# Performance work log

Measured on AMD Instinct MI355X. Metric: run time of the kernel, lower is better.

The kernel has to match this reference:

```python
import jax, jax.numpy as jnp
import numpy as np

WS = 8      # window size
NH = 8      # num heads
SCALE = 4.0 # qk_scale=4 from module defaults
GK = 9      # gaze depthwise kernel (nw=8 even -> 9)
EPS = 1e-5


def _rel_pos_index(ws):
    coords = np.stack(np.meshgrid(np.arange(ws), np.arange(ws), indexing='ij'))
    cf = coords.reshape(2, -1)
    rel = (cf[:, :, None] - cf[:, None, :]).transpose(1, 2, 0).astype(np.int64)
    rel[..., 0] += ws - 1
    rel[..., 1] += ws - 1
    rel[..., 0] *= 2 * ws - 1
    return jnp.asarray(rel.sum(-1))  # (N, N)


def _ln(x, g, b):
    m = x.mean(-1, keepdims=True)
    v = ((x - m) ** 2).mean(-1, keepdims=True)
    return (x - m) / jnp.sqrt(v + EPS) * g + b


def _forward(x, norm1_g, norm1_b, qkv_w, qkv_b, rpb_table, proj_w, proj_b,
             gaze_w, gaze_b, norm2_g, norm2_b, fc1_w, fc1_b, fc2_w, fc2_b, H, W):
    B, C, _, _ = x.shape
    hd = C // NH
    nw = H // WS           # windows per side (= Fold dilation)
    N = WS * WS            # tokens per window
    xf = x.transpose(0, 2, 3, 1).reshape(B, H * W, C)
    shortcut = xf
    xn = _ln(xf, norm1_g, norm1_b).reshape(B, H, W, C)
    # window partition -> (B*nw*nw, N, C)
    xw = xn.reshape(B, nw, WS, nw, WS, C).transpose(0, 1, 3, 2, 4, 5).reshape(B * nw * nw, N, C)
    qkv = (xw @ qkv_w.T + qkv_b).reshape(-1, N, 3, NH, hd).transpose(2, 0, 3, 1, 4)
    q, k, v = qkv[0] * SCALE, qkv[1], qkv[2]
    attn = jnp.einsum('whnd,whmd->whnm', q, k)  # (nWin, heads, N, N)
    rpi = _rel_pos_index(WS)
    bias = rpb_table[rpi.reshape(-1)].reshape(N, N, NH).transpose(2, 0, 1)
    attn = jax.nn.softmax(attn + bias[None], axis=-1)
    out = jnp.einsum('whnm,whmd->whnd', attn, v).transpose(0, 2, 1, 3).reshape(-1, N, C)
    # gaze branch: Fold (dilated scatter of windows into image), depthwise conv, Unfold
    v6 = v.reshape(B, nw, nw, NH, WS, WS, hd)          # (B, wh, ww, nh, i, j, hd)
    img = v6.transpose(0, 4, 1, 5, 2, 3, 6).reshape(B, H, W, C)  # row = i*nw+wh, col = j*nw+ww
    pad = GK // 2
    img = jax.lax.conv_general_dilated(
        img, gaze_w, (1, 1), ((pad, pad), (pad, pad)),
        dimension_numbers=('NHWC', 'HWIO', 'NHWC'), feature_group_count=C) + gaze_b
    gz = img.reshape(B, WS, nw, WS, nw, C).transpose(0, 2, 4, 1, 3, 5).reshape(B * nw * nw, N, C)
    out = (out + gz) @ proj_w.T + proj_b
    # window reverse -> (B, H*W, C)
    xr = out.reshape(B, nw, nw, WS, WS, C).transpose(0, 1, 3, 2, 4, 5).reshape(B, H * W, C)
    xf = shortcut + xr
    h = _ln(xf, norm2_g, norm2_b)
    h = jax.nn.gelu(h @ fc1_w.T + fc1_b, approximate=False) @ fc2_w.T + fc2_b
    xf = xf + h
    return xf.reshape(B, H, W, C).transpose(0, 3, 1, 2)


def setup_inputs() -> dict:
    key = jax.random.key(0)
    ks = jax.random.split(key, 8)
    C, H, W, B, HID = 256, 64, 64, 16, 1024
    return {
        'H': 64, 'W': 64,
        'x': jax.random.normal(ks[0], (B, C, H, W), jnp.float32),
        'norm1_g': jnp.ones((C,), jnp.float32),
        'norm1_b': jnp.zeros((C,), jnp.float32),
        'qkv_w': jax.random.normal(ks[1], (3 * C, C), jnp.float32) * 0.02,
        'qkv_b': jnp.zeros((3 * C,), jnp.float32),
        'rpb_table': jax.random.normal(ks[2], (225, NH), jnp.float32) * 0.02,
        'proj_w': jax.random.normal(ks[3], (C, C), jnp.float32) * 0.02,
        'proj_b': jnp.zeros((C,), jnp.float32),
        'gaze_w': jax.random.normal(ks[4], (GK, GK, 1, C), jnp.float32) * 0.02,
        'gaze_b': jnp.zeros((C,), jnp.float32),
        'norm2_g': jnp.ones((C,), jnp.float32),
        'norm2_b': jnp.zeros((C,), jnp.float32),
        'fc1_w': jax.random.normal(ks[5], (HID, C), jnp.float32) * 0.02,
        'fc1_b': jnp.zeros((HID,), jnp.float32),
        'fc2_w': jax.random.normal(ks[6], (C, HID), jnp.float32) * 0.02,
        'fc2_b': jnp.zeros((C,), jnp.float32),
    }


def reference(H, W, x, norm1_g, norm1_b, qkv_w, qkv_b, rpb_table, proj_w, proj_b,
              gaze_w, gaze_b, norm2_g, norm2_b, fc1_w, fc1_b, fc2_w, fc2_b):
    return _forward(x, norm1_g, norm1_b, qkv_w, qkv_b, rpb_table, proj_w, proj_b,
                    gaze_w, gaze_b, norm2_g, norm2_b, fc1_w, fc1_b, fc2_w, fc2_b, H, W)
```

## Files before the change

kernel.cpp:

```cpp
#include <hip/hip_runtime.h>
#include <math.h>

#define BB    16
#define CC    256
#define HH    64
#define WW2   64
#define NHD   8
#define HD    32
#define NT    64
#define NWIN  1024
#define TOK   65536
#define HIDN  1024
#define GKS   9
#define GPAD  4

typedef short bf16x8 __attribute__((ext_vector_type(8)));
typedef float f32x4  __attribute__((ext_vector_type(4)));
typedef unsigned short u16x8 __attribute__((ext_vector_type(8)));

__device__ __forceinline__ float b2f(unsigned short u) {
    return __uint_as_float(((unsigned int)u) << 16);
}
__device__ __forceinline__ unsigned short f2b(float f) {
    unsigned int x = __float_as_uint(f);
    unsigned int r = x + 0x7fffu + ((x >> 16) & 1u);
    return (unsigned short)(r >> 16);
}

__device__ __forceinline__ float gelu_f(float v) {
    const float c = 0.7978845608028654f;
    const float u = c * v * (1.0f + 0.044715f * v * v);
    const float e = __builtin_amdgcn_exp2f(2.8853900817779268f * u);
    const float t = 1.0f - 2.0f * __builtin_amdgcn_rcpf(e + 1.0f);
    return 0.5f * v * (1.0f + t);
}

#define O_N1G  64
#define O_N1B  320
#define O_QKVW 576
#define O_QKVB 197184
#define O_RPB  197952
#define O_PW   199808
#define O_PB   265344
#define O_GW   265600
#define O_GB   286336
#define O_N2G  286592
#define O_N2B  286848
#define O_W1   287104
#define O_B1   549248
#define O_W2   550272
#define O_B2   812416

struct ParTab {
    const void* src[15];
    int n[15];
    int off[15];
};

__global__ __launch_bounds__(256) void k_detect(const unsigned short* __restrict__ x,
                                                int* __restrict__ flag) {
    __shared__ int cnt;
    if (threadIdx.x == 0) cnt = 0;
    __syncthreads();
    const unsigned short u = x[threadIdx.x];
    const int e = (u >> 7) & 0xFF;
    if (e >= 140) atomicAdd(&cnt, 1);
    __syncthreads();
    if (threadIdx.x == 0) *flag = (cnt >= 8) ? 1 : 0;
}

__global__ __launch_bounds__(256) void k_conv_par(ParTab tab,
                                                  const int* __restrict__ flag,
                                                  unsigned short* __restrict__ par) {
    const int t = blockIdx.y;
    const int n = tab.n[t], off = tab.off[t];
    const bool f32 = (*flag != 0);
    for (int i = blockIdx.x * 256 + threadIdx.x; i < n; i += 64 * 256) {
        par[off + i] = f32 ? f2b(((const float*)tab.src[t])[i])
                           : ((const unsigned short*)tab.src[t])[i];
    }
}

__global__ __launch_bounds__(256) void k_pre(const void* __restrict__ xsrc,
                                             const int* __restrict__ flag,
                                             const unsigned short* __restrict__ g,
                                             const unsigned short* __restrict__ bt,
                                             unsigned short* __restrict__ SC,
                                             unsigned short* __restrict__ XN) {
    __shared__ __align__(16) unsigned short xs[256 * 65];
    __shared__ float ps[4][64], ps2[4][64];
    __shared__ float mean_s[64], rstd_s[64];
    const int tid = threadIdx.x;
    const int win = blockIdx.x;
    const int b = win >> 6, wh = (win >> 3) & 7, ww = win & 7;
    const bool f32 = (*flag != 0);

    for (int idx = tid; idx < 16384; idx += 256) {
        const int c = idx >> 6, n = idx & 63;
        const int h = wh * 8 + (n >> 3), w = ww * 8 + (n & 7);
        const size_t o = ((size_t)(b * CC + c) * HH + h) * WW2 + w;
        xs[c * 65 + n] = f32 ? f2b(((const float*)xsrc)[o])
                             : ((const unsigned short*)xsrc)[o];
    }
    __syncthreads();
    {
        const int tok = tid & 63, part = tid >> 6;
        float s = 0.f, s2 = 0.f;
        for (int c = part * 64; c < part * 64 + 64; ++c) {
            const float v = b2f(xs[c * 65 + tok]);
            s += v; s2 += v * v;
        }
        ps[part][tok] = s; ps2[part][tok] = s2;
    }
    __syncthreads();
    if (tid < 64) {
        const float s  = ps[0][tid] + ps[1][tid] + ps[2][tid] + ps[3][tid];
        const float s2 = ps2[0][tid] + ps2[1][tid] + ps2[2][tid] + ps2[3][tid];
        const float mean = s * (1.f / 256.f);
        const float var  = s2 * (1.f / 256.f) - mean * mean;
        mean_s[tid] = mean;
        rstd_s[tid] = rsqrtf(var + 1e-5f);
    }
    __syncthreads();
    for (int idx = tid; idx < 16384; idx += 256) {
        const int n = idx >> 8, c = idx & 255;
        const unsigned short raw = xs[c * 65 + n];
        const float v = (b2f(raw) - mean_s[n]) * rstd_s[n] * b2f(g[c]) + b2f(bt[c]);
        const size_t o = (size_t)(win * NT + n) * CC + c;
        SC[o] = raw;
        XN[o] = f2b(v);
    }
}

template <int KDIM, typename PreF, typename PostF>
__device__ __forceinline__ void gemm128(const unsigned short* __restrict__ A,
                                        const unsigned short* __restrict__ Bw,
                                        PreF pre, PostF post8) {
    __shared__ __align__(16) unsigned short smem[128 * 136];
    unsigned short* As = smem;
    unsigned short* Bs = smem + 8192;
    const int tid = threadIdx.x;
    const int wv = tid >> 6, ln = tid & 63;
    const int wm = wv & 1, wn = wv >> 1;
    const int m0 = blockIdx.x * 128, n0 = blockIdx.y * 128;

    f32x4 acc[4][4] = {};

    const int u = tid;

    for (int kb = 0; kb < KDIM; kb += 64) {
#pragma unroll
        for (int i = 0; i < 4; ++i) {
            const int uu = i * 256 + u;
            const int row = uu >> 3;
            const int c8 = ((uu & 7) ^ (row & 7)) * 8;
            __builtin_amdgcn_global_load_lds(
                (const __attribute__((address_space(1))) unsigned int*)
                    &A[(size_t)(m0 + row) * KDIM + kb + c8],
                (__attribute__((address_space(3))) unsigned int*)&As[uu * 8],
                16, 0, 0);
            __builtin_amdgcn_global_load_lds(
                (const __attribute__((address_space(1))) unsigned int*)
                    &Bw[(size_t)(n0 + row) * KDIM + kb + c8],
                (__attribute__((address_space(3))) unsigned int*)&Bs[uu * 8],
                16, 0, 0);
        }
        __syncthreads();
#pragma unroll
        for (int ks = 0; ks < 2; ++ks) {
            bf16x8 af[4], bf[4];
            const int sl = ks * 4 + (ln >> 4);
#pragma unroll
            for (int t = 0; t < 4; ++t) {
                const int ra = wm * 64 + t * 16 + (ln & 15);
                const int rb = wn * 64 + t * 16 + (ln & 15);
                af[t] = *(const bf16x8*)&As[ra * 64 + ((sl ^ (ra & 7)) * 8)];
                bf[t] = *(const bf16x8*)&Bs[rb * 64 + ((sl ^ (rb & 7)) * 8)];
            }
#pragma unroll
            for (int mt = 0; mt < 4; ++mt)
#pragma unroll
                for (int nt = 0; nt < 4; ++nt)
                    acc[mt][nt] = __builtin_amdgcn_mfma_f32_16x16x32_bf16(af[mt], bf[nt], acc[mt][nt], 0, 0, 0);
        }
        __syncthreads();
    }

    unsigned short* Cs = smem;
#pragma unroll
    for (int mt = 0; mt < 4; ++mt)
#pragma unroll
        for (int nt = 0; nt < 4; ++nt)
#pragma unroll
            for (int r = 0; r < 4; ++r) {
                const int ml = wm * 64 + mt * 16 + (ln >> 4) * 4 + r;
                const int nl = wn * 64 + nt * 16 + (ln & 15);
                Cs[ml * 136 + nl] = f2b(pre(m0 + ml, n0 + nl, acc[mt][nt][r]));
            }
    __syncthreads();
#pragma unroll
    for (int i = 0; i < 8; ++i) {
        const int j = i * 256 + tid;
        const int row = j >> 4, c8 = (j & 15) * 8;
        const u16x8 vals = *(const u16x8*)&Cs[row * 136 + c8];
        post8(m0 + row, n0 + c8, vals);
    }
}

__global__ __launch_bounds__(256) void k_gemm_qkv(const unsigned short* __restrict__ XN,
                                                  const unsigned short* __restrict__ Wq,
                                                  const unsigned short* __restrict__ bq,
                                                  unsigned short* __restrict__ Q,
                                                  unsigned short* __restrict__ K,
                                                  unsigned short* __restrict__ V) {
    gemm128<256>(XN, Wq,
        [&](int m, int n, float v) {
            v += b2f(bq[n]);
            return (n < 256) ? v * 4.0f : v;
        },
        [&](int m, int nb, u16x8 vals) {
            unsigned short* dst = (nb < 256) ? Q : ((nb < 512) ? K : V);
            *(u16x8*)&dst[(size_t)m * CC + (nb & 255)] = vals;
        });
}

__global__ __launch_bounds__(256) void k_attn(const unsigned short* __restrict__ Q,
                                              const unsigned short* __restrict__ K,
                                              const unsigned short* __restrict__ V,
                                              const unsigned short* __restrict__ rpb,
                                              unsigned short* __restrict__ AO) {
    __shared__ __align__(16) unsigned short Pb[64 * 72];
    __shared__ __align__(16) unsigned short Vt[32 * 72];
    const int tid = threadIdx.x, wv = tid >> 6, ln = tid & 63;
    const int win = blockIdx.x, head = blockIdx.y;
    const size_t tbase = (size_t)(win * NT) * CC + head * HD;

    for (int idx = tid; idx < 2048; idx += 256) {
        const int tok = idx >> 5, d = idx & 31;
        Vt[d * 72 + tok] = V[tbase + (size_t)tok * CC + d];
    }

    const bf16x8 a = *(const bf16x8*)&Q[tbase + (size_t)(16 * wv + (ln & 15)) * CC + (ln >> 4) * 8];
    f32x4 accs[4] = {};
#pragma unroll
    for (int f = 0; f < 4; ++f) {
        const bf16x8 b = *(const bf16x8*)&K[tbase + (size_t)(f * 16 + (ln & 15)) * CC + (ln >> 4) * 8];
        accs[f] = __builtin_amdgcn_mfma_f32_16x16x32_bf16(a, b, accs[f], 0, 0, 0);
    }
    const int qloc = (ln >> 4) * 4;
#pragma unroll
    for (int f = 0; f < 4; ++f)
#pragma unroll
        for (int r = 0; r < 4; ++r) {
            const int rr = 16 * wv + qloc + r;
            const int cth = f * 16 + (ln & 15);
            const int bidx = ((rr >> 3) - (cth >> 3) + 7) * 15 + ((rr & 7) - (cth & 7) + 7);
            accs[f][r] += b2f(rpb[bidx * NHD + head]);
        }
#pragma unroll
    for (int r = 0; r < 4; ++r) {
        float m = fmaxf(fmaxf(accs[0][r], accs[1][r]), fmaxf(accs[2][r], accs[3][r]));
#pragma unroll
        for (int o = 1; o <= 8; o <<= 1) m = fmaxf(m, __shfl_xor(m, o));
        float p[4], s = 0.f;
#pragma unroll
        for (int f = 0; f < 4; ++f) { p[f] = expf(accs[f][r] - m); s += p[f]; }
#pragma unroll
        for (int o = 1; o <= 8; o <<= 1) s += __shfl_xor(s, o);
        const float inv = 1.f / s;
#pragma unroll
        for (int f = 0; f < 4; ++f)
            Pb[(16 * wv + qloc + r) * 72 + f * 16 + (ln & 15)] = f2b(p[f] * inv);
    }
    __syncthreads();

    f32x4 acco[2] = {};
#pragma unroll
    for (int kb = 0; kb < 64; kb += 32) {
        const bf16x8 ap = *(const bf16x8*)&Pb[(16 * wv + (ln & 15)) * 72 + kb + (ln >> 4) * 8];
#pragma unroll
        for (int f = 0; f < 2; ++f) {
            const bf16x8 bv = *(const bf16x8*)&Vt[(f * 16 + (ln & 15)) * 72 + kb + (ln >> 4) * 8];
            acco[f] = __builtin_amdgcn_mfma_f32_16x16x32_bf16(ap, bv, acco[f], 0, 0, 0);
        }
    }
#pragma unroll
    for (int f = 0; f < 2; ++f)
#pragma unroll
        for (int r = 0; r < 4; ++r) {
            const int rr = 16 * wv + qloc + r;
            const int d = f * 16 + (ln & 15);
            AO[tbase + (size_t)rr * CC + d] = f2b(acco[f][r]);
        }
}

__global__ __launch_bounds__(256) void k_gaze(const unsigned short* __restrict__ V,
                                              const unsigned short* __restrict__ gw,
                                              const unsigned short* __restrict__ gb,
                                              unsigned short* __restrict__ AO) {
    __shared__ __align__(16) unsigned short ins[24 * 16 * 32];
    __shared__ __align__(16) unsigned short wlds[81 * 32];
    const int tid = threadIdx.x;
    const int c0 = blockIdx.x * 8, r0 = blockIdx.y * 16;
    const int b = blockIdx.z >> 3, head = blockIdx.z & 7;

    for (int idx = tid; idx < 1536; idx += 256) {
        const int pix = idx >> 2, v4 = (idx & 3) * 8;
        const int row = pix >> 4, colL = pix & 15;
        const int rp = r0 + row - GPAD, cp = c0 + colL - GPAD;
        uint4 val = {0, 0, 0, 0};
        if (rp >= 0 && rp < HH && cp >= 0 && cp < WW2) {
            const int win = b * 64 + (rp & 7) * 8 + (cp & 7);
            const int n = (rp >> 3) * 8 + (cp >> 3);
            val = *(const uint4*)&V[(size_t)(win * NT + n) * CC + head * HD + v4];
        }
        *(uint4*)&ins[(row * 16 + colL) * 32 + v4] = val;
    }
    for (int idx = tid; idx < 324; idx += 256) {
        const int k = idx >> 2, v4 = (idx & 3) * 8;
        *(uint4*)&wlds[k * 32 + v4] = *(const uint4*)&gw[k * CC + head * HD + v4];
    }
    __syncthreads();

    const int d = tid & 31;
    const int col = tid >> 5;
    float out[16];
#pragma unroll
    for (int ro = 0; ro < 16; ++ro) out[ro] = 0.f;

#pragma unroll
    for (int dx = 0; dx < GKS; ++dx) {
        float wreg[GKS];
#pragma unroll
        for (int dy = 0; dy < GKS; ++dy)
            wreg[dy] = b2f(wlds[(dy * GKS + dx) * 32 + d]);
        float inreg[24];
#pragma unroll
        for (int ri = 0; ri < 24; ++ri)
            inreg[ri] = b2f(ins[(ri * 16 + col + dx) * 32 + d]);
#pragma unroll
        for (int ro = 0; ro < 16; ++ro)
#pragma unroll
            for (int dy = 0; dy < GKS; ++dy)
                out[ro] = fmaf(inreg[ro + dy], wreg[dy], out[ro]);
    }

    const float bias = b2f(gb[head * HD + d]);
    const int c = c0 + col;
#pragma unroll
    for (int ro = 0; ro < 16; ++ro) {
        const int r = r0 + ro;
        const int win0 = b * 64 + (r & 7) * 8 + (c & 7);
        const int n0 = (r >> 3) * 8 + (c >> 3);
        const size_t o = (size_t)(win0 * NT + n0) * CC + head * HD + d;
        AO[o] = f2b(b2f(AO[o]) + out[ro] + bias);
    }
}

__global__ __launch_bounds__(256) void k_gemm_proj(const unsigned short* __restrict__ AO,
                                                   const unsigned short* __restrict__ Wp,
                                                   const unsigned short* __restrict__ bp,
                                                   const unsigned short* __restrict__ SC,
                                                   unsigned short* __restrict__ X2) {
    gemm128<256>(AO, Wp,
        [&](int m, int n, float v) { return v + b2f(bp[n]); },
        [&](int m, int nb, u16x8 vals) {
            const u16x8 sc = *(const u16x8*)&SC[(size_t)m * CC + nb];
            u16x8 o;
#pragma unroll
            for (int j = 0; j < 8; ++j) o[j] = f2b(b2f(vals[j]) + b2f(sc[j]));
            *(u16x8*)&X2[(size_t)m * CC + nb] = o;
        });
}

__global__ __launch_bounds__(256) void k_ln2(const unsigned short* __restrict__ X2,
                                             const unsigned short* __restrict__ g,
                                             const unsigned short* __restrict__ bt,
                                             unsigned short* __restrict__ X2N) {
    const int wv = threadIdx.x >> 6, ln = threadIdx.x & 63;
    const int t = blockIdx.x * 4 + wv;
    float vals[4];
    float s = 0.f, s2 = 0.f;
#pragma unroll
    for (int k = 0; k < 4; ++k) {
        const float v = b2f(X2[(size_t)t * CC + k * 64 + ln]);
        vals[k] = v; s += v; s2 += v * v;
    }
#pragma unroll
    for (int off = 32; off; off >>= 1) {
        s += __shfl_xor(s, off);
        s2 += __shfl_xor(s2, off);
    }
    const float mean = s * (1.f / 256.f);
    const float rstd = rsqrtf(s2 * (1.f / 256.f) - mean * mean + 1e-5f);
#pragma unroll
    for (int k = 0; k < 4; ++k) {
        const int c = k * 64 + ln;
        X2N[(size_t)t * CC + c] = f2b((vals[k] - mean) * rstd * b2f(g[c]) + b2f(bt[c]));
    }
}

__global__ __launch_bounds__(256) void k_gemm_fc1(const unsigned short* __restrict__ X2N,
                                                  const unsigned short* __restrict__ W1,
                                                  const unsigned short* __restrict__ b1,
                                                  unsigned short* __restrict__ H1) {
    gemm128<256>(X2N, W1,
        [&](int m, int n, float v) {
            v += b2f(b1[n]);
            return gelu_f(v);
        },
        [&](int m, int nb, u16x8 vals) {
            *(u16x8*)&H1[(size_t)m * HIDN + nb] = vals;
        });
}

__global__ __launch_bounds__(256) void k_gemm_fc2(const unsigned short* __restrict__ H1,
                                                  const unsigned short* __restrict__ W2,
                                                  const unsigned short* __restrict__ b2v,
                                                  const unsigned short* __restrict__ X2,
                                                  unsigned short* __restrict__ XOUT) {
    gemm128<1024>(H1, W2,
        [&](int m, int n, float v) { return v + b2f(b2v[n]); },
        [&](int m, int nb, u16x8 vals) {
            const u16x8 r = *(const u16x8*)&X2[(size_t)m * CC + nb];
            u16x8 o;
#pragma unroll
            for (int j = 0; j < 8; ++j) o[j] = f2b(b2f(vals[j]) + b2f(r[j]));
            *(u16x8*)&XOUT[(size_t)m * CC + nb] = o;
        });
}

__global__ __launch_bounds__(256) void k_out(const unsigned short* __restrict__ XOUT,
                                             const int* __restrict__ flag,
                                             void* __restrict__ out) {
    __shared__ __align__(16) unsigned short ys[64 * 257];
    const int tid = threadIdx.x;
    const int win = blockIdx.x;
    const int b = win >> 6, wh = (win >> 3) & 7, ww = win & 7;
    for (int idx = tid; idx < 16384; idx += 256) {
        const int n = idx >> 8, c = idx & 255;
        ys[n * 257 + c] = XOUT[(size_t)(win * NT + n) * CC + c];
    }
    __syncthreads();
    const bool f32 = (*flag != 0);
    for (int idx = tid; idx < 16384; idx += 256) {
        const int ch = idx >> 6, n = idx & 63;
        const int h = wh * 8 + (n >> 3), w = ww * 8 + (n & 7);
        const size_t o = ((size_t)(b * CC + ch) * HH + h) * WW2 + w;
        const unsigned short v = ys[n * 257 + ch];
        if (f32) ((float*)out)[o] = b2f(v);
        else     ((unsigned short*)out)[o] = v;
    }
}

extern "C" void kernel_launch(void* const* d_in, const int* in_sizes, int n_in,
                              void* d_out, int out_size, void* d_ws, size_t ws_size,
                              hipStream_t stream) {
    char* ws = (char*)d_ws;
    const size_t MB = 1048576;
    unsigned short* SC  = (unsigned short*)(ws);
    unsigned short* XN  = (unsigned short*)(ws + 32 * MB);
    unsigned short* Qb  = (unsigned short*)(ws + 64 * MB);
    unsigned short* Kb  = (unsigned short*)(ws + 96 * MB);
    unsigned short* Vb  = (unsigned short*)(ws + 128 * MB);
    unsigned short* AO  = (unsigned short*)(ws + 160 * MB);
    unsigned short* H1  = (unsigned short*)(ws + 64 * MB);
    unsigned short* X2  = (unsigned short*)(ws + 192 * MB);
    unsigned short* PAR = (unsigned short*)(ws + 224 * MB);
    int* FLAG = (int*)(ws + 224 * MB);
    unsigned short* X2N  = XN;
    unsigned short* XOUT = XN;

    ParTab tab;
    const int srcidx[15] = {3, 4, 5, 6, 7, 8, 9, 10, 11, 12, 13, 14, 15, 16, 17};
    const int sizes[15]  = {256, 256, 196608, 768, 1800, 65536, 256, 20736, 256,
                            256, 256, 262144, 1024, 262144, 256};
    const int offs[15]   = {O_N1G, O_N1B, O_QKVW, O_QKVB, O_RPB, O_PW, O_PB, O_GW, O_GB,
                            O_N2G, O_N2B, O_W1, O_B1, O_W2, O_B2};
    for (int i = 0; i < 15; ++i) {
        tab.src[i] = d_in[srcidx[i]];
        tab.n[i] = sizes[i];
        tab.off[i] = offs[i];
    }

    k_detect   <<<1,                 256, 0, stream>>>((const unsigned short*)d_in[2], FLAG);
    k_conv_par <<<dim3(64, 15),      256, 0, stream>>>(tab, FLAG, PAR);
    k_pre      <<<NWIN,              256, 0, stream>>>(d_in[2], FLAG, PAR + O_N1G, PAR + O_N1B, SC, XN);
    k_gemm_qkv <<<dim3(512, 6),      256, 0, stream>>>(XN, PAR + O_QKVW, PAR + O_QKVB, Qb, Kb, Vb);
    k_attn     <<<dim3(NWIN, NHD),   256, 0, stream>>>(Qb, Kb, Vb, PAR + O_RPB, AO);
    k_gaze     <<<dim3(8, 4, 128),   256, 0, stream>>>(Vb, PAR + O_GW, PAR + O_GB, AO);
    k_gemm_proj<<<dim3(512, 2),      256, 0, stream>>>(AO, PAR + O_PW, PAR + O_PB, SC, X2);
    k_ln2      <<<TOK / 4,           256, 0, stream>>>(X2, PAR + O_N2G, PAR + O_N2B, X2N);
    k_gemm_fc1 <<<dim3(512, 8),      256, 0, stream>>>(X2N, PAR + O_W1, PAR + O_B1, H1);
    k_gemm_fc2 <<<dim3(512, 2),      256, 0, stream>>>(H1, PAR + O_W2, PAR + O_B2, X2, XOUT);
    k_out      <<<NWIN,              256, 0, stream>>>(XOUT, FLAG, d_out);
}
```

Before: 587.5 us.

## Fold qk scale into weights, hoist GEMM bias, swap grid order, vectorize LN2

Pre-multiplies the Q rows of the QKV weights and bias by the scale during parameter conversion, so the GEMM epilogue no longer multiplies. Hoists the bias load into registers per wave, uses packed v_cvt_pk_bf16 conversions, and uses a cheaper sigmoid-form GELU approximation. Swaps the GEMM grid so the N tiles vary fastest, which should improve reuse of the A tile in L2. Vectorizes the V transpose load in attention and the LN2 kernel to 16-byte accesses. Pre-scaling in bf16 rounds slightly differently, and the GELU form changes numerics a little.

```diff
diff --git a/kernel.cpp b/kernel.cpp
--- a/kernel.cpp
+++ b/kernel.cpp
@@ -26,13 +26,29 @@
     unsigned int r = x + 0x7fffu + ((x >> 16) & 1u);
     return (unsigned short)(r >> 16);
 }
+__device__ __forceinline__ unsigned int cvt_pk_bf16(float lo, float hi) {
+    unsigned int r;
+    asm("v_cvt_pk_bf16_f32 %0, %1, %2" : "=v"(r) : "v"(lo), "v"(hi));
+    return r;
+}
 
 __device__ __forceinline__ float gelu_f(float v) {
-    const float c = 0.7978845608028654f;
-    const float u = c * v * (1.0f + 0.044715f * v * v);
-    const float e = __builtin_amdgcn_exp2f(2.8853900817779268f * u);
-    const float t = 1.0f - 2.0f * __builtin_amdgcn_rcpf(e + 1.0f);
-    return 0.5f * v * (1.0f + t);
+    const float w = v * v;
+    const float u = v * fmaf(w, -0.1029432f, -2.3022082f);
+    const float e = __builtin_amdgcn_exp2f(u);
+    return v * __builtin_amdgcn_rcpf(1.0f + e);
+}
+
+__device__ __forceinline__ u16x8 add_bf8(u16x8 a, u16x8 b) {
+    u16x8 o;
+#pragma unroll
+    for (int j = 0; j < 8; j += 2) {
+        const unsigned int p = cvt_pk_bf16(b2f(a[j]) + b2f(b[j]),
+                                           b2f(a[j + 1]) + b2f(b[j + 1]));
+        o[j] = (unsigned short)p;
+        o[j + 1] = (unsigned short)(p >> 16);
+    }
+    return o;
 }
 
 #define O_N1G  64
@@ -75,9 +91,19 @@
     const int t = blockIdx.y;
     const int n = tab.n[t], off = tab.off[t];
     const bool f32 = (*flag != 0);
+    const bool scaled = (t == 2) || (t == 3);
+    const int slim = (t == 2) ? 65536 : 256;
     for (int i = blockIdx.x * 256 + threadIdx.x; i < n; i += 64 * 256) {
-        par[off + i] = f32 ? f2b(((const float*)tab.src[t])[i])
-                           : ((const unsigned short*)tab.src[t])[i];
+        unsigned short r;
+        if (f32) {
+            float v = ((const float*)tab.src[t])[i];
+            if (scaled && i < slim) v *= 4.0f;
+            r = f2b(v);
+        } else {
+            r = ((const unsigned short*)tab.src[t])[i];
+            if (scaled && i < slim) r = f2b(b2f(r) * 4.0f);
+        }
+        par[off + i] = r;
     }
 }
 
@@ -132,20 +158,25 @@
     }
 }
 
-template <int KDIM, typename PreF, typename PostF>
+template <int KDIM, int ACT, typename PostF>
 __device__ __forceinline__ void gemm128(const unsigned short* __restrict__ A,
                                         const unsigned short* __restrict__ Bw,
-                                        PreF pre, PostF post8) {
+                                        const unsigned short* __restrict__ bias,
+                                        PostF post8) {
     __shared__ __align__(16) unsigned short smem[128 * 136];
     unsigned short* As = smem;
     unsigned short* Bs = smem + 8192;
     const int tid = threadIdx.x;
     const int wv = tid >> 6, ln = tid & 63;
     const int wm = wv & 1, wn = wv >> 1;
-    const int m0 = blockIdx.x * 128, n0 = blockIdx.y * 128;
+    const int m0 = blockIdx.y * 128, n0 = blockIdx.x * 128;
+
+    float bias_v[4];
+#pragma unroll
+    for (int nt = 0; nt < 4; ++nt)
+        bias_v[nt] = b2f(bias[n0 + wn * 64 + nt * 16 + (ln & 15)]);
 
     f32x4 acc[4][4] = {};
-
     const int u = tid;
 
     for (int kb = 0; kb < KDIM; kb += 64) {
@@ -190,13 +221,23 @@
 #pragma unroll
     for (int mt = 0; mt < 4; ++mt)
 #pragma unroll
-        for (int nt = 0; nt < 4; ++nt)
+        for (int nt = 0; nt < 4; ++nt) {
+            float v[4];
 #pragma unroll
             for (int r = 0; r < 4; ++r) {
-                const int ml = wm * 64 + mt * 16 + (ln >> 4) * 4 + r;
-                const int nl = wn * 64 + nt * 16 + (ln & 15);
-                Cs[ml * 136 + nl] = f2b(pre(m0 + ml, n0 + nl, acc[mt][nt][r]));
+                float x = acc[mt][nt][r] + bias_v[nt];
+                if (ACT == 1) x = gelu_f(x);
+                v[r] = x;
             }
+            const int mlb = wm * 64 + mt * 16 + (ln >> 4) * 4;
+            const int nl = wn * 64 + nt * 16 + (ln & 15);
+            const unsigned int p0 = cvt_pk_bf16(v[0], v[1]);
+            const unsigned int p1 = cvt_pk_bf16(v[2], v[3]);
+            Cs[(mlb + 0) * 136 + nl] = (unsigned short)p0;
+            Cs[(mlb + 1) * 136 + nl] = (unsigned short)(p0 >> 16);
+            Cs[(mlb + 2) * 136 + nl] = (unsigned short)p1;
+            Cs[(mlb + 3) * 136 + nl] = (unsigned short)(p1 >> 16);
+        }
     __syncthreads();
 #pragma unroll
     for (int i = 0; i < 8; ++i) {
@@ -213,11 +254,7 @@
                                                   unsigned short* __restrict__ Q,
                                                   unsigned short* __restrict__ K,
                                                   unsigned short* __restrict__ V) {
-    gemm128<256>(XN, Wq,
-        [&](int m, int n, float v) {
-            v += b2f(bq[n]);
-            return (n < 256) ? v * 4.0f : v;
-        },
+    gemm128<256, 0>(XN, Wq, bq,
         [&](int m, int nb, u16x8 vals) {
             unsigned short* dst = (nb < 256) ? Q : ((nb < 512) ? K : V);
             *(u16x8*)&dst[(size_t)m * CC + (nb & 255)] = vals;
@@ -235,9 +272,11 @@
     const int win = blockIdx.x, head = blockIdx.y;
     const size_t tbase = (size_t)(win * NT) * CC + head * HD;
 
-    for (int idx = tid; idx < 2048; idx += 256) {
-        const int tok = idx >> 5, d = idx & 31;
-        Vt[d * 72 + tok] = V[tbase + (size_t)tok * CC + d];
+    {
+        const int tok = tid >> 2, d8 = (tid & 3) * 8;
+        const u16x8 vv = *(const u16x8*)&V[tbase + (size_t)tok * CC + d8];
+#pragma unroll
+        for (int j = 0; j < 8; ++j) Vt[(d8 + j) * 72 + tok] = vv[j];
     }
 
     const bf16x8 a = *(const bf16x8*)&Q[tbase + (size_t)(16 * wv + (ln & 15)) * CC + (ln >> 4) * 8];
@@ -362,14 +401,10 @@
                                                    const unsigned short* __restrict__ bp,
                                                    const unsigned short* __restrict__ SC,
                                                    unsigned short* __restrict__ X2) {
-    gemm128<256>(AO, Wp,
-        [&](int m, int n, float v) { return v + b2f(bp[n]); },
+    gemm128<256, 0>(AO, Wp, bp,
         [&](int m, int nb, u16x8 vals) {
             const u16x8 sc = *(const u16x8*)&SC[(size_t)m * CC + nb];
-            u16x8 o;
-#pragma unroll
-            for (int j = 0; j < 8; ++j) o[j] = f2b(b2f(vals[j]) + b2f(sc[j]));
-            *(u16x8*)&X2[(size_t)m * CC + nb] = o;
+            *(u16x8*)&X2[(size_t)m * CC + nb] = add_bf8(vals, sc);
         });
 }
 
@@ -377,38 +412,44 @@
                                              const unsigned short* __restrict__ g,
                                              const unsigned short* __restrict__ bt,
                                              unsigned short* __restrict__ X2N) {
-    const int wv = threadIdx.x >> 6, ln = threadIdx.x & 63;
-    const int t = blockIdx.x * 4 + wv;
-    float vals[4];
+    const int tid = threadIdx.x;
+    const int wv = tid >> 6, ln = tid & 63;
+    const int t = blockIdx.x * 8 + wv * 2 + (ln >> 5);
+    const int c8 = (ln & 31) * 8;
+    const u16x8 xv = *(const u16x8*)&X2[(size_t)t * CC + c8];
+    float vals[8];
     float s = 0.f, s2 = 0.f;
 #pragma unroll
-    for (int k = 0; k < 4; ++k) {
-        const float v = b2f(X2[(size_t)t * CC + k * 64 + ln]);
-        vals[k] = v; s += v; s2 += v * v;
-    }
-#pragma unroll
-    for (int off = 32; off; off >>= 1) {
+    for (int j = 0; j < 8; ++j) {
+        const float v = b2f(xv[j]);
+        vals[j] = v; s += v; s2 += v * v;
+    }
+#pragma unroll
+    for (int off = 16; off; off >>= 1) {
         s += __shfl_xor(s, off);
         s2 += __shfl_xor(s2, off);
     }
     const float mean = s * (1.f / 256.f);
     const float rstd = rsqrtf(s2 * (1.f / 256.f) - mean * mean + 1e-5f);
-#pragma unroll
-    for (int k = 0; k < 4; ++k) {
-        const int c = k * 64 + ln;
-        X2N[(size_t)t * CC + c] = f2b((vals[k] - mean) * rstd * b2f(g[c]) + b2f(bt[c]));
-    }
+    const u16x8 gv = *(const u16x8*)&g[c8];
+    const u16x8 bv = *(const u16x8*)&bt[c8];
+    u16x8 o;
+#pragma unroll
+    for (int j = 0; j < 8; j += 2) {
+        const float a0 = (vals[j] - mean) * rstd * b2f(gv[j]) + b2f(bv[j]);
+        const float a1 = (vals[j + 1] - mean) * rstd * b2f(gv[j + 1]) + b2f(bv[j + 1]);
+        const unsigned int p = cvt_pk_bf16(a0, a1);
+        o[j] = (unsigned short)p;
+        o[j + 1] = (unsigned short)(p >> 16);
+    }
+    *(u16x8*)&X2N[(size_t)t * CC + c8] = o;
 }
 
 __global__ __launch_bounds__(256) void k_gemm_fc1(const unsigned short* __restrict__ X2N,
                                                   const unsigned short* __restrict__ W1,
                                                   const unsigned short* __restrict__ b1,
                                                   unsigned short* __restrict__ H1) {
-    gemm128<256>(X2N, W1,
-        [&](int m, int n, float v) {
-            v += b2f(b1[n]);
-            return gelu_f(v);
-        },
+    gemm128<256, 1>(X2N, W1, b1,
         [&](int m, int nb, u16x8 vals) {
             *(u16x8*)&H1[(size_t)m * HIDN + nb] = vals;
         });
@@ -419,14 +460,10 @@
                                                   const unsigned short* __restrict__ b2v,
                                                   const unsigned short* __restrict__ X2,
                                                   unsigned short* __restrict__ XOUT) {
-    gemm128<1024>(H1, W2,
-        [&](int m, int n, float v) { return v + b2f(b2v[n]); },
+    gemm128<1024, 0>(H1, W2, b2v,
         [&](int m, int nb, u16x8 vals) {
             const u16x8 r = *(const u16x8*)&X2[(size_t)m * CC + nb];
-            u16x8 o;
-#pragma unroll
-            for (int j = 0; j < 8; ++j) o[j] = f2b(b2f(vals[j]) + b2f(r[j]));
-            *(u16x8*)&XOUT[(size_t)m * CC + nb] = o;
+            *(u16x8*)&XOUT[(size_t)m * CC + nb] = add_bf8(vals, r);
         });
 }
 
@@ -486,12 +523,12 @@
     k_detect   <<<1,                 256, 0, stream>>>((const unsigned short*)d_in[2], FLAG);
     k_conv_par <<<dim3(64, 15),      256, 0, stream>>>(tab, FLAG, PAR);
     k_pre      <<<NWIN,              256, 0, stream>>>(d_in[2], FLAG, PAR + O_N1G, PAR + O_N1B, SC, XN);
-    k_gemm_qkv <<<dim3(512, 6),      256, 0, stream>>>(XN, PAR + O_QKVW, PAR + O_QKVB, Qb, Kb, Vb);
+    k_gemm_qkv <<<dim3(6, 512),      256, 0, stream>>>(XN, PAR + O_QKVW, PAR + O_QKVB, Qb, Kb, Vb);
     k_attn     <<<dim3(NWIN, NHD),   256, 0, stream>>>(Qb, Kb, Vb, PAR + O_RPB, AO);
     k_gaze     <<<dim3(8, 4, 128),   256, 0, stream>>>(Vb, PAR + O_GW, PAR + O_GB, AO);
-    k_gemm_proj<<<dim3(512, 2),      256, 0, stream>>>(AO, PAR + O_PW, PAR + O_PB, SC, X2);
-    k_ln2      <<<TOK / 4,           256, 0, stream>>>(X2, PAR + O_N2G, PAR + O_N2B, X2N);
-    k_gemm_fc1 <<<dim3(512, 8),      256, 0, stream>>>(X2N, PAR + O_W1, PAR + O_B1, H1);
-    k_gemm_fc2 <<<dim3(512, 2),      256, 0, stream>>>(H1, PAR + O_W2, PAR + O_B2, X2, XOUT);
+    k_gemm_proj<<<dim3(2, 512),      256, 0, stream>>>(AO, PAR + O_PW, PAR + O_PB, SC, X2);
+    k_ln2      <<<TOK / 8,           256, 0, stream>>>(X2, PAR + O_N2G, PAR + O_N2B, X2N);
+    k_gemm_fc1 <<<dim3(8, 512),      256, 0, stream>>>(X2N, PAR + O_W1, PAR + O_B1, H1);
+    k_gemm_fc2 <<<dim3(2, 512),      256, 0, stream>>>(H1, PAR + O_W2, PAR + O_B2, X2, XOUT);
     k_out      <<<NWIN,              256, 0, stream>>>(XOUT, FLAG, d_out);
 }
```

New measurement: 543.6 us. 7.5% less time.
